# Optimization experiments

Hardware: AMD Instinct MI355X
Metric: run time of the kernel (lower is better)

Reference implementation:

```python
import jax, jax.numpy as jnp
import numpy as np


def setup_inputs() -> dict:
    key = jax.random.key(0)
    B, N, C = 16, 4096, 768  # SAM ViT-B token tensor [batch, tokens, channels]
    x = jax.random.normal(key, (B, N, C), dtype=jnp.float32)
    k = 384        # int(C * p2) with p2 = 0.5
    largest = 1    # torch.topk largest=True
    return {"x": x, "k": k, "largest": largest}


def reference(x, k, largest):
    # torch.topk(x, k, dim=2, largest=largest) with dim=2 == last axis for 3D x,
    # then scatter values back into zeros_like(x) at the selected indices.
    if largest:
        vals, idx = jax.lax.top_k(x, k)            # [B, N, k]
    else:
        neg_vals, idx = jax.lax.top_k(-x, k)
        vals = -neg_vals
    B, N, _ = x.shape
    b = jnp.arange(B)[:, None, None]               # broadcast batch index
    n = jnp.arange(N)[None, :, None]               # broadcast token index
    out = jnp.zeros_like(x).at[b, n, idx].set(vals)
    return out
```

## Files before the change

### kernel.cpp

```cpp
#include <hip/hip_runtime.h>
#include <cstdint>


constexpr int C   = 768;
constexpr int TPB = 256;
constexpr int WPB = TPB / 64;
constexpr int EPL = C / 64;
constexpr int NV  = EPL / 4;
constexpr int RPW = 8;

typedef uint32_t uint4v  __attribute__((ext_vector_type(4)));
typedef float    float4v __attribute__((ext_vector_type(4)));

__device__ __forceinline__ uint32_t f2key(uint32_t b, uint32_t flip) {
    uint32_t m = (uint32_t)((int32_t)b >> 31) | 0x80000000u;
    return (b ^ m) ^ flip;
}
__device__ __forceinline__ float key2f(uint32_t key, uint32_t flip) {
    uint32_t u = key ^ flip;
    uint32_t m = (~(uint32_t)((int32_t)u >> 31)) | 0x80000000u;
    return __uint_as_float(u ^ m);
}

__global__ __launch_bounds__(TPB, 8) void topk_scatter_row(
        const float* __restrict__ x,
        const int*   __restrict__ pk,
        const int*   __restrict__ plg,
        float*       __restrict__ out,
        int rows) {
    const int lane = threadIdx.x & 63;
    const int wid  = threadIdx.x >> 6;
    const int row0 = (blockIdx.x * WPB + wid) * RPW;
    if (row0 >= rows) return;

    const int      k    = pk[0];
    const uint32_t flip = (plg[0] != 0) ? 0u : 0xFFFFFFFFu;

    const uint4v* xv = (const uint4v*)(x + (size_t)row0 * C);
    const int nrow = (rows - row0 < RPW) ? (rows - row0) : RPW;

    uint4v pre[NV];
    #pragma unroll
    for (int j = 0; j < NV; ++j)
        pre[j] = __builtin_nontemporal_load(&xv[j * 64 + lane]);

    for (int i = 0; i < nrow; ++i) {
        uint32_t key[EPL];
        #pragma unroll
        for (int j = 0; j < NV; ++j) {
            #pragma unroll
            for (int c2 = 0; c2 < 4; ++c2)
                key[j*4+c2] = f2key(pre[j][c2], flip);
        }
        if (i + 1 < nrow) {
            const uint4v* xn = xv + (size_t)(i + 1) * (C / 4);
            #pragma unroll
            for (int j = 0; j < NV; ++j)
                pre[j] = __builtin_nontemporal_load(&xn[j * 64 + lane]);
        }

        float4v* orow = (float4v*)(out + (size_t)(row0 + i) * C);

        if (k <= 0) {
            const float4v z = {0.f, 0.f, 0.f, 0.f};
            #pragma unroll
            for (int j = 0; j < NV; ++j)
                __builtin_nontemporal_store(z, &orow[j * 64 + lane]);
            continue;
        }
        if (k >= C) {
            #pragma unroll
            for (int j = 0; j < NV; ++j) {
                float4v o;
                #pragma unroll
                for (int c2 = 0; c2 < 4; ++c2) o[c2] = key2f(key[j*4+c2], flip);
                __builtin_nontemporal_store(o, &orow[j * 64 + lane]);
            }
            continue;
        }

        uint32_t T = 0;
        bool exact = false;
        for (int b = 31; b >= 0; --b) {
            const uint32_t cand = T | (1u << b);
            int cnt = 0;
            #pragma unroll
            for (int e = 0; e < EPL; ++e)
                cnt += __popcll(__ballot(key[e] >= cand));
            if (cnt >= k) {
                T = cand;
                if (cnt == k) { exact = true; break; }
            }
        }

        uint32_t selmask = 0;
        if (exact) {
            #pragma unroll
            for (int e = 0; e < EPL; ++e)
                if (key[e] >= T) selmask |= 1u << e;
        } else {
            int cgt = 0;
            #pragma unroll
            for (int e = 0; e < EPL; ++e) {
                if (key[e] > T) selmask |= 1u << e;
                cgt += __popcll(__ballot(key[e] > T));
            }
            const int need = k - cgt;
            const unsigned long long below = (1ull << lane) - 1ull;
            int base = 0;
            #pragma unroll
            for (int j = 0; j < NV; ++j) {
                int eq[4]; unsigned long long m[4];
                #pragma unroll
                for (int c2 = 0; c2 < 4; ++c2) {
                    eq[c2] = (key[j*4+c2] == T) ? 1 : 0;
                    m[c2]  = __ballot(eq[c2] != 0);
                }
                int lanebelow = 0;
                #pragma unroll
                for (int c2 = 0; c2 < 4; ++c2) lanebelow += __popcll(m[c2] & below);
                int own = 0;
                #pragma unroll
                for (int c2 = 0; c2 < 4; ++c2) {
                    if (eq[c2] && (base + lanebelow + own) < need)
                        selmask |= 1u << (j*4 + c2);
                    own += eq[c2];
                }
                #pragma unroll
                for (int c2 = 0; c2 < 4; ++c2) base += __popcll(m[c2]);
            }
        }

        #pragma unroll
        for (int j = 0; j < NV; ++j) {
            float4v o;
            #pragma unroll
            for (int c2 = 0; c2 < 4; ++c2) {
                const int e = j*4 + c2;
                o[c2] = ((selmask >> e) & 1u) ? key2f(key[e], flip) : 0.0f;
            }
            __builtin_nontemporal_store(o, &orow[j * 64 + lane]);
        }
    }
}

extern "C" void kernel_launch(void* const* d_in, const int* in_sizes, int n_in,
                              void* d_out, int out_size, void* d_ws, size_t ws_size,
                              hipStream_t stream) {
    const float* x   = (const float*)d_in[0];
    const int*   pk  = (const int*)d_in[1];
    const int*   plg = (const int*)d_in[2];
    float*       out = (float*)d_out;

    const int rows      = in_sizes[0] / C;
    const int rows_blk  = WPB * RPW;
    const int blocks    = (rows + rows_blk - 1) / rows_blk;
    topk_scatter_row<<<blocks, TPB, 0, stream>>>(x, pk, plg, out, rows);
}
```

Baseline: 346.6 us.

## Use grid-stride row loop with fixed grid and plain loads/stores

Rows are no longer split into fixed contiguous chunks of 8 per wave. Each wave now walks rows with a grid stride across a fixed grid of 4096 blocks and prefetches the next strided row. Nontemporal loads and stores become ordinary ones, and the occupancy hint in launch_bounds is dropped. The aim is better load balance and latency hiding across the GPU, at the cost of losing the streaming cache hints and contiguous per-wave row access.

```diff
diff --git a/kernel.cpp b/kernel.cpp
--- a/kernel.cpp
+++ b/kernel.cpp
@@ -7,7 +7,6 @@
 constexpr int WPB = TPB / 64;
 constexpr int EPL = C / 64;
 constexpr int NV  = EPL / 4;
-constexpr int RPW = 8;
 
 typedef uint32_t uint4v  __attribute__((ext_vector_type(4)));
 typedef float    float4v __attribute__((ext_vector_type(4)));
@@ -22,29 +21,30 @@
     return __uint_as_float(u ^ m);
 }
 
-__global__ __launch_bounds__(TPB, 8) void topk_scatter_row(
+__global__ __launch_bounds__(TPB) void topk_scatter_row(
         const float* __restrict__ x,
         const int*   __restrict__ pk,
         const int*   __restrict__ plg,
         float*       __restrict__ out,
         int rows) {
-    const int lane = threadIdx.x & 63;
-    const int wid  = threadIdx.x >> 6;
-    const int row0 = (blockIdx.x * WPB + wid) * RPW;
-    if (row0 >= rows) return;
+    const int lane   = threadIdx.x & 63;
+    const int wave   = blockIdx.x * WPB + (threadIdx.x >> 6);
+    const int nwaves = gridDim.x * WPB;
 
     const int      k    = pk[0];
     const uint32_t flip = (plg[0] != 0) ? 0u : 0xFFFFFFFFu;
 
-    const uint4v* xv = (const uint4v*)(x + (size_t)row0 * C);
-    const int nrow = (rows - row0 < RPW) ? (rows - row0) : RPW;
+    int row = wave;
+    if (row >= rows) return;
 
     uint4v pre[NV];
-    #pragma unroll
-    for (int j = 0; j < NV; ++j)
-        pre[j] = __builtin_nontemporal_load(&xv[j * 64 + lane]);
+    {
+        const uint4v* xr = (const uint4v*)(x + (size_t)row * C);
+        #pragma unroll
+        for (int j = 0; j < NV; ++j) pre[j] = xr[j * 64 + lane];
+    }
 
-    for (int i = 0; i < nrow; ++i) {
+    for (; row < rows; row += nwaves) {
         uint32_t key[EPL];
         #pragma unroll
         for (int j = 0; j < NV; ++j) {
@@ -52,20 +52,19 @@
             for (int c2 = 0; c2 < 4; ++c2)
                 key[j*4+c2] = f2key(pre[j][c2], flip);
         }
-        if (i + 1 < nrow) {
-            const uint4v* xn = xv + (size_t)(i + 1) * (C / 4);
+        const int nxt = row + nwaves;
+        if (nxt < rows) {
+            const uint4v* xn = (const uint4v*)(x + (size_t)nxt * C);
             #pragma unroll
-            for (int j = 0; j < NV; ++j)
-                pre[j] = __builtin_nontemporal_load(&xn[j * 64 + lane]);
+            for (int j = 0; j < NV; ++j) pre[j] = xn[j * 64 + lane];
         }
 
-        float4v* orow = (float4v*)(out + (size_t)(row0 + i) * C);
+        float4v* orow = (float4v*)(out + (size_t)row * C);
 
         if (k <= 0) {
             const float4v z = {0.f, 0.f, 0.f, 0.f};
             #pragma unroll
-            for (int j = 0; j < NV; ++j)
-                __builtin_nontemporal_store(z, &orow[j * 64 + lane]);
+            for (int j = 0; j < NV; ++j) orow[j * 64 + lane] = z;
             continue;
         }
         if (k >= C) {
@@ -74,7 +73,7 @@
                 float4v o;
                 #pragma unroll
                 for (int c2 = 0; c2 < 4; ++c2) o[c2] = key2f(key[j*4+c2], flip);
-                __builtin_nontemporal_store(o, &orow[j * 64 + lane]);
+                orow[j * 64 + lane] = o;
             }
             continue;
         }
@@ -139,7 +138,7 @@
                 const int e = j*4 + c2;
                 o[c2] = ((selmask >> e) & 1u) ? key2f(key[e], flip) : 0.0f;
             }
-            __builtin_nontemporal_store(o, &orow[j * 64 + lane]);
+            orow[j * 64 + lane] = o;
         }
     }
 }
@@ -152,8 +151,7 @@
     const int*   plg = (const int*)d_in[2];
     float*       out = (float*)d_out;
 
-    const int rows      = in_sizes[0] / C;
-    const int rows_blk  = WPB * RPW;
-    const int blocks    = (rows + rows_blk - 1) / rows_blk;
+    const int rows   = in_sizes[0] / C;
+    const int blocks = 4096;
     topk_scatter_row<<<blocks, TPB, 0, stream>>>(x, pk, plg, out, rows);
 }
```

Result: no change. 342.5 us (-1.2%).
